# Optimization experiments

Measured on AMD Instinct MI355X. Metric: run time of the kernel, lower is better.

Reference implementation:

```python
import jax, jax.numpy as jnp
import numpy as np

V, D = 100000, 128
B, Q, C, T = 1024, 64, 64, 8


def setup_inputs() -> dict:
    key = jax.random.key(0)
    ks = jax.random.split(key, 9)
    embed = jax.random.normal(ks[0], (V, D), dtype=jnp.float32) * 0.1
    embed = embed.at[0].set(0.0)  # padding_idx=0
    q_ids = jax.random.randint(ks[1], (B, Q), 1, V)
    c_ids = jax.random.randint(ks[2], (B, C, T), 1, V)
    num_qs = jax.random.randint(ks[3], (B,), 1, Q + 1)
    num_cols = jax.random.randint(ks[4], (B,), 1, C + 1)
    W_h = jax.random.normal(ks[5], (5 * D, D), dtype=jnp.float32) * 0.02
    b_h = jnp.zeros((D,), jnp.float32)
    W_o = jax.random.normal(ks[6], (D, 1), dtype=jnp.float32) * 0.02
    b_o = jnp.zeros((1,), jnp.float32)
    return {"q_ids": q_ids, "c_ids": c_ids, "num_qs": num_qs, "num_cols": num_cols,
            "embed": embed, "W_h": W_h, "b_h": b_h, "W_o": W_o, "b_o": b_o}


def _forward(q_ids, c_ids, num_qs, num_cols, embed, W_h, b_h, W_o, b_o):
    d = embed.shape[1]
    # ColumnSummarizer: pad-masked mean over column tokens -> [B, C, D]
    c_tok = embed[c_ids]                       # [B, C, T, D]
    c_mask = (c_ids != 0).astype(c_tok.dtype)  # [B, C, T]
    denom = jnp.maximum(c_mask.sum(-1, keepdims=True), 1.0)
    c_h = (c_tok * c_mask[..., None]).sum(-2) / denom  # [B, C, D]
    # QuestionSummarizer: q_h = token embeddings, q_summary = length-masked mean
    q_h = embed[q_ids]                         # [B, Q, D]
    q_valid = (jnp.arange(q_h.shape[1])[None, :] < num_qs[:, None])  # [B, Q]
    qv = q_valid.astype(q_h.dtype)
    q_summary = (q_h * qv[..., None]).sum(1) / jnp.maximum(
        num_qs[:, None].astype(q_h.dtype), 1.0)  # [B, D]
    # scaled dot-product attention, columns attend over question tokens
    sim = jnp.einsum('bcd,bqd->bcq', c_h, q_h) / jnp.sqrt(jnp.asarray(d, c_h.dtype))
    sim = jnp.where(q_valid[:, None, :], sim, -jnp.inf)  # mask padded q tokens
    att = jax.nn.softmax(sim, axis=-1)                    # [B, C, Q]
    weighted_q = jnp.einsum('bcq,bqd->bcd', att, q_h)     # [B, C, D]
    q_tiled = jnp.broadcast_to(q_summary[:, None, :], c_h.shape)
    feats = jnp.concatenate(
        [q_tiled, c_h, weighted_q, c_h * weighted_q, jnp.abs(c_h - weighted_q)],
        axis=-1)                                           # [B, C, 5D]
    h = jnp.tanh(feats @ W_h + b_h)
    return h @ W_o + b_o                                   # [B, C, 1]


def reference(q_ids, c_ids, num_qs, num_cols, embed, W_h, b_h, W_o, b_o):
    return _forward(q_ids, c_ids, num_qs, num_cols, embed, W_h, b_h, W_o, b_o)
```

## Files before the change

### kernel.cpp

```cpp
#include <hip/hip_runtime.h>


typedef __attribute__((ext_vector_type(8))) short     short8;
typedef __attribute__((ext_vector_type(8))) __bf16    bf16x8;
typedef __attribute__((ext_vector_type(4))) float     f32x4;
typedef __attribute__((ext_vector_type(4))) int       int4v;

#define SWZ8(row, off) ((off) ^ (((row) & 7) << 4))
#define SWZQ(row, off) ((off) ^ (((row) & 7) << 4) ^ ((((row) >> 3) & 3) << 5))

#define CH_OFF  0
#define QH_OFF  16384
#define X_OFF   32768
#define LDS_SIZE 40960

__device__ __forceinline__ unsigned short f2bf(float x) {
    __bf16 h = (__bf16)x;
    return __builtin_bit_cast(unsigned short, h);
}
__device__ __forceinline__ float bf2f(unsigned short u) {
    return __builtin_bit_cast(float, ((unsigned)u) << 16);
}
__device__ __forceinline__ float bflo(unsigned u) {
    return __builtin_bit_cast(float, u << 16);
}
__device__ __forceinline__ float bfhi(unsigned u) {
    return __builtin_bit_cast(float, u & 0xFFFF0000u);
}
__device__ __forceinline__ unsigned pk2(float a, float b) {
    return (unsigned)f2bf(a) | ((unsigned)f2bf(b) << 16);
}
__device__ __forceinline__ f32x4 mfma16(short8 a, short8 b, f32x4 c) {
    return __builtin_amdgcn_mfma_f32_16x16x32_bf16(
        __builtin_bit_cast(bf16x8, a), __builtin_bit_cast(bf16x8, b), c, 0, 0, 0);
}

__global__ __launch_bounds__(256) void el_prep(const float* __restrict__ W_h,
                                               unsigned short* __restrict__ whT) {
    int t = blockIdx.x * 256 + threadIdx.x;
    int k = t >> 7, n = t & 127;
    whT[n * 640 + k] = f2bf(W_h[t]);
}

__global__ __launch_bounds__(256) void el_conv(const float* __restrict__ e,
                                               unsigned short* __restrict__ ebf) {
    long i = ((long)blockIdx.x * 256 + threadIdx.x) * 8;
    f32x4 a = *(const f32x4*)(e + i);
    f32x4 c = *(const f32x4*)(e + i + 4);
    uint4 pk;
    pk.x = pk2(a[0], a[1]); pk.y = pk2(a[2], a[3]);
    pk.z = pk2(c[0], c[1]); pk.w = pk2(c[2], c[3]);
    *(uint4*)(ebf + i) = pk;
}

template <bool BF16E>
__global__ __launch_bounds__(256, 4) void el_main(
    const int* __restrict__ q_ids, const int* __restrict__ c_ids,
    const int* __restrict__ num_qs, const float* __restrict__ emb,
    const unsigned short* __restrict__ ebf,
    const unsigned short* __restrict__ whT,
    unsigned short* __restrict__ qsum_ws,
    const float* __restrict__ b_h,
    const float* __restrict__ W_o, const float* __restrict__ b_o,
    float* __restrict__ out)
{
    __shared__ __align__(16) char smem[LDS_SIZE];
    const int tid = threadIdx.x;
    const int b = blockIdx.x;
    const int nq = num_qs[b] > 0 ? num_qs[b] : 1;

    {
        const int l4 = tid & 15, gg = tid >> 4;
        #pragma unroll 2
        for (int cc = 0; cc < 4; ++cc) {
            const int c = gg + cc * 16;
            const int* idp = c_ids + (((b << 6) + c) << 3);
            int4v i0 = *(const int4v*)idp, i1 = *(const int4v*)(idp + 4);
            int id8[8] = {i0[0], i0[1], i0[2], i0[3], i1[0], i1[1], i1[2], i1[3]};
            int cnt = 0;
            #pragma unroll
            for (int t = 0; t < 8; ++t) cnt += (id8[t] != 0);
            float acc[8] = {0.f,0.f,0.f,0.f,0.f,0.f,0.f,0.f};
            #pragma unroll
            for (int t = 0; t < 8; ++t) {
                if constexpr (BF16E) {
                    uint4 v = *(const uint4*)(ebf + (long)id8[t] * 128 + l4 * 8);
                    acc[0] += bflo(v.x); acc[1] += bfhi(v.x);
                    acc[2] += bflo(v.y); acc[3] += bfhi(v.y);
                    acc[4] += bflo(v.z); acc[5] += bfhi(v.z);
                    acc[6] += bflo(v.w); acc[7] += bfhi(v.w);
                } else {
                    f32x4 lo = *(const f32x4*)(emb + (long)id8[t] * 128 + l4 * 8);
                    f32x4 hi = *(const f32x4*)(emb + (long)id8[t] * 128 + l4 * 8 + 4);
                    acc[0] += lo[0]; acc[1] += lo[1]; acc[2] += lo[2]; acc[3] += lo[3];
                    acc[4] += hi[0]; acc[5] += hi[1]; acc[6] += hi[2]; acc[7] += hi[3];
                }
            }
            float inv = 1.0f / (float)(cnt > 0 ? cnt : 1);
            uint4 pk;
            pk.x = pk2(acc[0]*inv, acc[1]*inv); pk.y = pk2(acc[2]*inv, acc[3]*inv);
            pk.z = pk2(acc[4]*inv, acc[5]*inv); pk.w = pk2(acc[6]*inv, acc[7]*inv);
            *(uint4*)(smem + CH_OFF + SWZ8(c, c * 256 + l4 * 16)) = pk;
        }
        float qa[8] = {0.f,0.f,0.f,0.f,0.f,0.f,0.f,0.f};
        #pragma unroll
        for (int qq = 0; qq < 4; ++qq) {
            const int q = gg + (qq << 4);
            int id = q_ids[(b << 6) + q];
            uint4 v;
            if constexpr (BF16E) {
                v = *(const uint4*)(ebf + (long)id * 128 + l4 * 8);
            } else {
                f32x4 lo = *(const f32x4*)(emb + (long)id * 128 + l4 * 8);
                f32x4 hi = *(const f32x4*)(emb + (long)id * 128 + l4 * 8 + 4);
                v.x = pk2(lo[0], lo[1]); v.y = pk2(lo[2], lo[3]);
                v.z = pk2(hi[0], hi[1]); v.w = pk2(hi[2], hi[3]);
            }
            *(uint4*)(smem + QH_OFF + SWZQ(q, q * 256 + l4 * 16)) = v;
            if (q < nq) {
                qa[0] += bflo(v.x); qa[1] += bfhi(v.x);
                qa[2] += bflo(v.y); qa[3] += bfhi(v.y);
                qa[4] += bflo(v.z); qa[5] += bfhi(v.z);
                qa[6] += bflo(v.w); qa[7] += bfhi(v.w);
            }
        }
        float* qsp = (float*)(smem + X_OFF);
        *(f32x4*)(qsp + gg * 128 + l4 * 8)     = (f32x4){qa[0], qa[1], qa[2], qa[3]};
        *(f32x4*)(qsp + gg * 128 + l4 * 8 + 4) = (f32x4){qa[4], qa[5], qa[6], qa[7]};
    }
    __syncthreads();

    if (tid < 128) {
        const float* qsp = (const float*)(smem + X_OFF);
        float s = 0.f;
        #pragma unroll
        for (int g = 0; g < 16; ++g) s += qsp[g * 128 + tid];
        qsum_ws[(b << 7) + tid] = f2bf(s / (float)nq);
    }
    __syncthreads();

    const int lane = tid & 63, w = tid >> 6;
    const int lr = lane & 15, lg = lane >> 4;

    {
        short8 a[4];
        const int arow = w * 16 + lr;
        #pragma unroll
        for (int s = 0; s < 4; ++s)
            a[s] = *(const short8*)(smem + CH_OFF + SWZ8(arow, arow * 256 + s * 64 + lg * 16));
        f32x4 sim[4];
        #pragma unroll
        for (int ct = 0; ct < 4; ++ct) {
            f32x4 acc = {0.f, 0.f, 0.f, 0.f};
            const int q = ct * 16 + lr;
            #pragma unroll
            for (int s = 0; s < 4; ++s) {
                short8 bf = *(const short8*)(smem + QH_OFF + SWZQ(q, q * 256 + s * 64 + lg * 16));
                acc = mfma16(a[s], bf, acc);
            }
            sim[ct] = acc;
        }
        const float scale = 0.08838834764831845f;
        #pragma unroll
        for (int ct = 0; ct < 4; ++ct) {
            const int q = ct * 16 + lr;
            #pragma unroll
            for (int r = 0; r < 4; ++r)
                sim[ct][r] = (q < nq) ? sim[ct][r] * scale : -3.0e38f;
        }
        float mx[4], sm[4];
        #pragma unroll
        for (int r = 0; r < 4; ++r)
            mx[r] = fmaxf(fmaxf(sim[0][r], sim[1][r]), fmaxf(sim[2][r], sim[3][r]));
        #pragma unroll
        for (int off = 1; off <= 8; off <<= 1)
            #pragma unroll
            for (int r = 0; r < 4; ++r)
                mx[r] = fmaxf(mx[r], __shfl_xor(mx[r], off));
        #pragma unroll
        for (int ct = 0; ct < 4; ++ct)
            #pragma unroll
            for (int r = 0; r < 4; ++r)
                sim[ct][r] = __expf(sim[ct][r] - mx[r]);
        #pragma unroll
        for (int r = 0; r < 4; ++r)
            sm[r] = (sim[0][r] + sim[1][r]) + (sim[2][r] + sim[3][r]);
        #pragma unroll
        for (int off = 1; off <= 8; off <<= 1)
            #pragma unroll
            for (int r = 0; r < 4; ++r)
                sm[r] += __shfl_xor(sm[r], off);
        const int cbase = w * 16 + lg * 4;
        #pragma unroll
        for (int ct = 0; ct < 4; ++ct)
            #pragma unroll
            for (int r = 0; r < 4; ++r) {
                int c = cbase + r, q = ct * 16 + lr;
                *(unsigned short*)(smem + X_OFF + SWZ8(c, c * 128 + q * 2)) =
                    f2bf(sim[ct][r] * (1.0f / sm[r]));
            }
    }
    __syncthreads();

    f32x4 wqa[8];
    {
        short8 pa[2];
        const int arow = w * 16 + lr;
        #pragma unroll
        for (int s = 0; s < 2; ++s)
            pa[s] = *(const short8*)(smem + X_OFF + SWZ8(arow, arow * 128 + s * 64 + lg * 16));
        #pragma unroll
        for (int ct = 0; ct < 8; ++ct) {
            f32x4 acc = {0.f, 0.f, 0.f, 0.f};
            const int d = ct * 16 + lr;
            const int dlx = (d << 1) ^ (lg << 5);
            #pragma unroll
            for (int s = 0; s < 2; ++s) {
                const int qbase = (s << 5) + (lg << 3);
                short8 bf;
                #pragma unroll
                for (int j = 0; j < 8; ++j) {
                    int off = QH_OFF + ((qbase + j) << 8) + (dlx ^ (j << 4));
                    bf[j] = *(const short*)(smem + off);
                }
                acc = mfma16(pa[s], bf, acc);
            }
            wqa[ct] = acc;
        }
    }
    __syncthreads();
    {
        const int cbase = w * 16 + lg * 4;
        #pragma unroll
        for (int ct = 0; ct < 8; ++ct)
            #pragma unroll
            for (int r = 0; r < 4; ++r) {
                int c = cbase + r, d = ct * 16 + lr;
                *(unsigned short*)(smem + QH_OFF + SWZQ(c, c * 256 + d * 2)) =
                    f2bf(wqa[ct][r]);
            }
    }
    __syncthreads();

    {
        f32x4 acc[4][2];
        #pragma unroll
        for (int rt = 0; rt < 4; ++rt) {
            acc[rt][0] = (f32x4){0.f, 0.f, 0.f, 0.f};
            acc[rt][1] = (f32x4){0.f, 0.f, 0.f, 0.f};
        }
        const int n0 = w * 32 + lr, n1 = n0 + 16;
        const int klane = lg * 8;
        short8 qsf[4];
        #pragma unroll
        for (int sk = 0; sk < 4; ++sk)
            qsf[sk] = *(const short8*)(qsum_ws + (b << 7) + sk * 32 + klane);
        const float bh0 = b_h[n0], bh1 = b_h[n1];
        const float wo0 = W_o[n0], wo1 = W_o[n1];

        for (int sk = 0; sk < 4; ++sk) {
            short8 B0[5], B1[5];
            #pragma unroll
            for (int p = 0; p < 5; ++p) {
                B0[p] = *(const short8*)(whT + n0 * 640 + p * 128 + sk * 32 + klane);
                B1[p] = *(const short8*)(whT + n1 * 640 + p * 128 + sk * 32 + klane);
            }
            #pragma unroll
            for (int rt = 0; rt < 4; ++rt) {
                const int row = rt * 16 + lr;
                short8 chf = *(const short8*)(smem + CH_OFF + SWZ8(row, row * 256 + sk * 64 + lg * 16));
                short8 wqf = *(const short8*)(smem + QH_OFF + SWZQ(row, row * 256 + sk * 64 + lg * 16));
                short8 prf, adf;
                #pragma unroll
                for (int e = 0; e < 8; ++e) {
                    float cv = bf2f((unsigned short)chf[e]);
                    float wv = bf2f((unsigned short)wqf[e]);
                    prf[e] = (short)f2bf(cv * wv);
                    adf[e] = (short)f2bf(fabsf(cv - wv));
                }
                acc[rt][0] = mfma16(qsf[sk], B0[0], acc[rt][0]);
                acc[rt][1] = mfma16(qsf[sk], B1[0], acc[rt][1]);
                acc[rt][0] = mfma16(chf,     B0[1], acc[rt][0]);
                acc[rt][1] = mfma16(chf,     B1[1], acc[rt][1]);
                acc[rt][0] = mfma16(wqf,     B0[2], acc[rt][0]);
                acc[rt][1] = mfma16(wqf,     B1[2], acc[rt][1]);
                acc[rt][0] = mfma16(prf,     B0[3], acc[rt][0]);
                acc[rt][1] = mfma16(prf,     B1[3], acc[rt][1]);
                acc[rt][0] = mfma16(adf,     B0[4], acc[rt][0]);
                acc[rt][1] = mfma16(adf,     B1[4], acc[rt][1]);
            }
        }

        #pragma unroll
        for (int rt = 0; rt < 4; ++rt)
            #pragma unroll
            for (int r = 0; r < 4; ++r) {
                float x0 = acc[rt][0][r] + bh0;
                float x1 = acc[rt][1][r] + bh1;
                float t0 = 1.0f - 2.0f / (__expf(2.0f * x0) + 1.0f);
                float t1 = 1.0f - 2.0f / (__expf(2.0f * x1) + 1.0f);
                float po = t0 * wo0 + t1 * wo1;
                #pragma unroll
                for (int off = 1; off <= 8; off <<= 1)
                    po += __shfl_xor(po, off);
                if (lr == 0)
                    *(float*)(smem + X_OFF + (w * 64 + rt * 16 + lg * 4 + r) * 4) = po;
            }
    }
    __syncthreads();

    if (tid < 64) {
        float o = b_o[0];
        #pragma unroll
        for (int w2 = 0; w2 < 4; ++w2)
            o += *(const float*)(smem + X_OFF + (w2 * 64 + tid) * 4);
        out[(b << 6) + tid] = o;
    }
}

extern "C" void kernel_launch(void* const* d_in, const int* in_sizes, int n_in,
                              void* d_out, int out_size, void* d_ws, size_t ws_size,
                              hipStream_t stream) {
    const int*   q_ids  = (const int*)d_in[0];
    const int*   c_ids  = (const int*)d_in[1];
    const int*   num_qs = (const int*)d_in[2];
    const float* embed  = (const float*)d_in[4];
    const float* W_h    = (const float*)d_in[5];
    const float* b_h    = (const float*)d_in[6];
    const float* W_o    = (const float*)d_in[7];
    const float* b_o    = (const float*)d_in[8];
    float*       out    = (float*)d_out;

    unsigned short* whT  = (unsigned short*)d_ws;
    unsigned short* qsum = (unsigned short*)((char*)d_ws + 163840);
    unsigned short* ebf  = (unsigned short*)((char*)d_ws + 425984);

    el_prep<<<320, 256, 0, stream>>>(W_h, whT);

    const bool bf16e = ws_size >= (size_t)(425984 + 100000 * 128 * 2);
    if (bf16e) {
        el_conv<<<6250, 256, 0, stream>>>(embed, ebf);
        el_main<true><<<1024, 256, 0, stream>>>(q_ids, c_ids, num_qs, embed, ebf,
                                                whT, qsum, b_h, W_o, b_o, out);
    } else {
        el_main<false><<<1024, 256, 0, stream>>>(q_ids, c_ids, num_qs, embed, ebf,
                                                 whT, qsum, b_h, W_o, b_o, out);
    }
}
```

Baseline: 151.2 us.

## Add main kernel variant staging attention probs in global workspace to cut LDS

Adds a new main kernel that writes the bf16 attention probabilities and partial question sums to a per-batch global workspace instead of LDS, which shrinks shared memory from 40 KB to 32 KB. It reuses the question-embedding LDS region for weighted_q, fuses the output projection with per-row atomicAdd into an output pre-initialised with b_o, and loads W_h fragments straight from global. The aim is more resident blocks per CU and fewer LDS round trips. In exchange it adds global-memory traffic, extra barriers and atomics, and it only runs when the workspace is large enough.

```diff
diff --git a/kernel.cpp b/kernel.cpp
--- a/kernel.cpp
+++ b/kernel.cpp
@@ -8,6 +8,10 @@
 
 #define SWZ8(row, off) ((off) ^ (((row) & 7) << 4))
 #define SWZQ(row, off) ((off) ^ (((row) & 7) << 4) ^ ((((row) >> 3) & 3) << 5))
+
+#define A_CH   0
+#define A_QH   16384
+#define A_LDS  32768
 
 #define CH_OFF  0
 #define QH_OFF  16384
@@ -53,8 +57,256 @@
     *(uint4*)(ebf + i) = pk;
 }
 
+__global__ __launch_bounds__(256, 4) void el_main_a(
+    const int* __restrict__ q_ids, const int* __restrict__ c_ids,
+    const int* __restrict__ num_qs,
+    const unsigned short* __restrict__ ebf,
+    const unsigned short* __restrict__ whT,
+    unsigned short* __restrict__ qsum_ws,
+    unsigned short* __restrict__ att_ws,
+    const float* __restrict__ b_h,
+    const float* __restrict__ W_o, const float* __restrict__ b_o,
+    float* __restrict__ out)
+{
+    __shared__ __align__(16) char smem[A_LDS];
+    const int tid = threadIdx.x;
+    const int b = blockIdx.x;
+    const int nq = num_qs[b] > 0 ? num_qs[b] : 1;
+    unsigned short* batt = att_ws + (size_t)b * 4096;
+    float* bqp = (float*)batt;
+
+    if (tid < 64) out[(b << 6) + tid] = b_o[0];
+
+    {
+        const int l4 = tid & 15, gg = tid >> 4;
+        #pragma unroll 2
+        for (int cc = 0; cc < 4; ++cc) {
+            const int c = gg + cc * 16;
+            const int* idp = c_ids + (((b << 6) + c) << 3);
+            int4v i0 = *(const int4v*)idp, i1 = *(const int4v*)(idp + 4);
+            int id8[8] = {i0[0], i0[1], i0[2], i0[3], i1[0], i1[1], i1[2], i1[3]};
+            int cnt = 0;
+            #pragma unroll
+            for (int t = 0; t < 8; ++t) cnt += (id8[t] != 0);
+            float acc[8] = {0.f,0.f,0.f,0.f,0.f,0.f,0.f,0.f};
+            #pragma unroll
+            for (int t = 0; t < 8; ++t) {
+                uint4 v = *(const uint4*)(ebf + (long)id8[t] * 128 + l4 * 8);
+                acc[0] += bflo(v.x); acc[1] += bfhi(v.x);
+                acc[2] += bflo(v.y); acc[3] += bfhi(v.y);
+                acc[4] += bflo(v.z); acc[5] += bfhi(v.z);
+                acc[6] += bflo(v.w); acc[7] += bfhi(v.w);
+            }
+            float inv = 1.0f / (float)(cnt > 0 ? cnt : 1);
+            uint4 pk;
+            pk.x = pk2(acc[0]*inv, acc[1]*inv); pk.y = pk2(acc[2]*inv, acc[3]*inv);
+            pk.z = pk2(acc[4]*inv, acc[5]*inv); pk.w = pk2(acc[6]*inv, acc[7]*inv);
+            *(uint4*)(smem + A_CH + SWZ8(c, c * 256 + l4 * 16)) = pk;
+        }
+        float qa[8] = {0.f,0.f,0.f,0.f,0.f,0.f,0.f,0.f};
+        #pragma unroll
+        for (int qq = 0; qq < 4; ++qq) {
+            const int q = gg + (qq << 4);
+            int id = q_ids[(b << 6) + q];
+            uint4 v = *(const uint4*)(ebf + (long)id * 128 + l4 * 8);
+            *(uint4*)(smem + A_QH + SWZQ(q, q * 256 + l4 * 16)) = v;
+            if (q < nq) {
+                qa[0] += bflo(v.x); qa[1] += bfhi(v.x);
+                qa[2] += bflo(v.y); qa[3] += bfhi(v.y);
+                qa[4] += bflo(v.z); qa[5] += bfhi(v.z);
+                qa[6] += bflo(v.w); qa[7] += bfhi(v.w);
+            }
+        }
+        #pragma unroll
+        for (int e = 0; e < 8; ++e) {
+            qa[e] += __shfl_xor(qa[e], 16);
+            qa[e] += __shfl_xor(qa[e], 32);
+        }
+        const int lane = tid & 63, w = tid >> 6;
+        if (lane < 16) {
+            *(f32x4*)(bqp + w * 128 + lane * 8)     = (f32x4){qa[0],qa[1],qa[2],qa[3]};
+            *(f32x4*)(bqp + w * 128 + lane * 8 + 4) = (f32x4){qa[4],qa[5],qa[6],qa[7]};
+        }
+    }
+    __syncthreads();
+
+    if (tid < 128) {
+        float s = bqp[tid] + bqp[128 + tid] + bqp[256 + tid] + bqp[384 + tid];
+        qsum_ws[(b << 7) + tid] = f2bf(s / (float)nq);
+    }
+    __syncthreads();
+
+    const int lane = tid & 63, w = tid >> 6;
+    const int lr = lane & 15, lg = lane >> 4;
+
+    {
+        short8 a[4];
+        const int arow = w * 16 + lr;
+        #pragma unroll
+        for (int s = 0; s < 4; ++s)
+            a[s] = *(const short8*)(smem + A_CH + SWZ8(arow, arow * 256 + s * 64 + lg * 16));
+        f32x4 sim[4];
+        #pragma unroll
+        for (int ct = 0; ct < 4; ++ct) {
+            f32x4 acc = {0.f, 0.f, 0.f, 0.f};
+            const int q = ct * 16 + lr;
+            #pragma unroll
+            for (int s = 0; s < 4; ++s) {
+                short8 bf = *(const short8*)(smem + A_QH + SWZQ(q, q * 256 + s * 64 + lg * 16));
+                acc = mfma16(a[s], bf, acc);
+            }
+            sim[ct] = acc;
+        }
+        const float scale = 0.08838834764831845f;
+        #pragma unroll
+        for (int ct = 0; ct < 4; ++ct) {
+            const int q = ct * 16 + lr;
+            #pragma unroll
+            for (int r = 0; r < 4; ++r)
+                sim[ct][r] = (q < nq) ? sim[ct][r] * scale : -3.0e38f;
+        }
+        float mx[4], sm[4];
+        #pragma unroll
+        for (int r = 0; r < 4; ++r)
+            mx[r] = fmaxf(fmaxf(sim[0][r], sim[1][r]), fmaxf(sim[2][r], sim[3][r]));
+        #pragma unroll
+        for (int off = 1; off <= 8; off <<= 1)
+            #pragma unroll
+            for (int r = 0; r < 4; ++r)
+                mx[r] = fmaxf(mx[r], __shfl_xor(mx[r], off));
+        #pragma unroll
+        for (int ct = 0; ct < 4; ++ct)
+            #pragma unroll
+            for (int r = 0; r < 4; ++r)
+                sim[ct][r] = __expf(sim[ct][r] - mx[r]);
+        #pragma unroll
+        for (int r = 0; r < 4; ++r)
+            sm[r] = (sim[0][r] + sim[1][r]) + (sim[2][r] + sim[3][r]);
+        #pragma unroll
+        for (int off = 1; off <= 8; off <<= 1)
+            #pragma unroll
+            for (int r = 0; r < 4; ++r)
+                sm[r] += __shfl_xor(sm[r], off);
+        const int cbase = w * 16 + lg * 4;
+        #pragma unroll
+        for (int ct = 0; ct < 4; ++ct)
+            #pragma unroll
+            for (int r = 0; r < 4; ++r) {
+                int c = cbase + r, q = ct * 16 + lr;
+                batt[c * 64 + q] = f2bf(sim[ct][r] * (1.0f / sm[r]));
+            }
+    }
+    __syncthreads();
+
+    f32x4 wqa[8];
+    {
+        short8 pa[2];
+        const int prow = w * 16 + lr;
+        #pragma unroll
+        for (int s = 0; s < 2; ++s)
+            pa[s] = *(const short8*)(batt + prow * 64 + s * 32 + lg * 8);
+        #pragma unroll
+        for (int ct = 0; ct < 8; ++ct) {
+            f32x4 acc = {0.f, 0.f, 0.f, 0.f};
+            const int d = ct * 16 + lr;
+            const int dlx = (d << 1) ^ (lg << 5);
+            #pragma unroll
+            for (int s = 0; s < 2; ++s) {
+                const int qbase = (s << 5) + (lg << 3);
+                short8 bf;
+                #pragma unroll
+                for (int j = 0; j < 8; ++j) {
+                    int off = A_QH + ((qbase + j) << 8) + (dlx ^ (j << 4));
+                    bf[j] = *(const short*)(smem + off);
+                }
+                acc = mfma16(pa[s], bf, acc);
+            }
+            wqa[ct] = acc;
+        }
+    }
+    __syncthreads();
+    {
+        const int cbase = w * 16 + lg * 4;
+        #pragma unroll
+        for (int ct = 0; ct < 8; ++ct)
+            #pragma unroll
+            for (int r = 0; r < 4; ++r) {
+                int c = cbase + r, d = ct * 16 + lr;
+                *(unsigned short*)(smem + A_QH + SWZQ(c, c * 256 + d * 2)) =
+                    f2bf(wqa[ct][r]);
+            }
+    }
+    __syncthreads();
+
+    {
+        f32x4 acc[4][2];
+        #pragma unroll
+        for (int rt = 0; rt < 4; ++rt) {
+            acc[rt][0] = (f32x4){0.f, 0.f, 0.f, 0.f};
+            acc[rt][1] = (f32x4){0.f, 0.f, 0.f, 0.f};
+        }
+        const int n0 = w * 32 + lr, n1 = n0 + 16;
+        const int klane = lg * 8;
+        short8 qsf[4];
+        #pragma unroll
+        for (int sk = 0; sk < 4; ++sk)
+            qsf[sk] = *(const short8*)(qsum_ws + (b << 7) + sk * 32 + klane);
+        const float bh0 = b_h[n0], bh1 = b_h[n1];
+        const float wo0 = W_o[n0], wo1 = W_o[n1];
+
+        for (int sk = 0; sk < 4; ++sk) {
+            short8 B0[5], B1[5];
+            #pragma unroll
+            for (int p = 0; p < 5; ++p) {
+                B0[p] = *(const short8*)(whT + n0 * 640 + p * 128 + sk * 32 + klane);
+                B1[p] = *(const short8*)(whT + n1 * 640 + p * 128 + sk * 32 + klane);
+            }
+            #pragma unroll
+            for (int rt = 0; rt < 4; ++rt) {
+                const int row = rt * 16 + lr;
+                short8 chf = *(const short8*)(smem + A_CH + SWZ8(row, row * 256 + sk * 64 + lg * 16));
+                short8 wqf = *(const short8*)(smem + A_QH + SWZQ(row, row * 256 + sk * 64 + lg * 16));
+                short8 prf, adf;
+                #pragma unroll
+                for (int e = 0; e < 8; ++e) {
+                    float cv = bf2f((unsigned short)chf[e]);
+                    float wv = bf2f((unsigned short)wqf[e]);
+                    prf[e] = (short)f2bf(cv * wv);
+                    adf[e] = (short)f2bf(fabsf(cv - wv));
+                }
+                acc[rt][0] = mfma16(qsf[sk], B0[0], acc[rt][0]);
+                acc[rt][1] = mfma16(qsf[sk], B1[0], acc[rt][1]);
+                acc[rt][0] = mfma16(chf,     B0[1], acc[rt][0]);
+                acc[rt][1] = mfma16(chf,     B1[1], acc[rt][1]);
+                acc[rt][0] = mfma16(wqf,     B0[2], acc[rt][0]);
+                acc[rt][1] = mfma16(wqf,     B1[2], acc[rt][1]);
+                acc[rt][0] = mfma16(prf,     B0[3], acc[rt][0]);
+                acc[rt][1] = mfma16(prf,     B1[3], acc[rt][1]);
+                acc[rt][0] = mfma16(adf,     B0[4], acc[rt][0]);
+                acc[rt][1] = mfma16(adf,     B1[4], acc[rt][1]);
+            }
+        }
+
+        #pragma unroll
+        for (int rt = 0; rt < 4; ++rt)
+            #pragma unroll
+            for (int r = 0; r < 4; ++r) {
+                float x0 = acc[rt][0][r] + bh0;
+                float x1 = acc[rt][1][r] + bh1;
+                float t0 = 1.0f - 2.0f / (__expf(2.0f * x0) + 1.0f);
+                float t1 = 1.0f - 2.0f / (__expf(2.0f * x1) + 1.0f);
+                float po = t0 * wo0 + t1 * wo1;
+                #pragma unroll
+                for (int off = 1; off <= 8; off <<= 1)
+                    po += __shfl_xor(po, off);
+                if (lr == 0)
+                    atomicAdd(out + (b << 6) + rt * 16 + lg * 4 + r, po);
+            }
+    }
+}
+
 template <bool BF16E>
-__global__ __launch_bounds__(256, 4) void el_main(
+__global__ __launch_bounds__(256, 4) void el_main_b(
     const int* __restrict__ q_ids, const int* __restrict__ c_ids,
     const int* __restrict__ num_qs, const float* __restrict__ emb,
     const unsigned short* __restrict__ ebf,
@@ -331,19 +583,26 @@
     const float* b_o    = (const float*)d_in[8];
     float*       out    = (float*)d_out;
 
+    const size_t EBF_OFF = 425984;
+    const size_t EBF_END = EBF_OFF + (size_t)100000 * 128 * 2;
+    const size_t ATT_END = EBF_END + (size_t)1024 * 4096 * 2;
     unsigned short* whT  = (unsigned short*)d_ws;
     unsigned short* qsum = (unsigned short*)((char*)d_ws + 163840);
-    unsigned short* ebf  = (unsigned short*)((char*)d_ws + 425984);
+    unsigned short* ebf  = (unsigned short*)((char*)d_ws + EBF_OFF);
+    unsigned short* attw = (unsigned short*)((char*)d_ws + EBF_END);
 
     el_prep<<<320, 256, 0, stream>>>(W_h, whT);
 
-    const bool bf16e = ws_size >= (size_t)(425984 + 100000 * 128 * 2);
-    if (bf16e) {
+    if (ws_size >= ATT_END) {
         el_conv<<<6250, 256, 0, stream>>>(embed, ebf);
-        el_main<true><<<1024, 256, 0, stream>>>(q_ids, c_ids, num_qs, embed, ebf,
-                                                whT, qsum, b_h, W_o, b_o, out);
+        el_main_a<<<1024, 256, 0, stream>>>(q_ids, c_ids, num_qs, ebf, whT,
+                                            qsum, attw, b_h, W_o, b_o, out);
+    } else if (ws_size >= EBF_END) {
+        el_conv<<<6250, 256, 0, stream>>>(embed, ebf);
+        el_main_b<true><<<1024, 256, 0, stream>>>(q_ids, c_ids, num_qs, embed, ebf,
+                                                  whT, qsum, b_h, W_o, b_o, out);
     } else {
-        el_main<false><<<1024, 256, 0, stream>>>(q_ids, c_ids, num_qs, embed, ebf,
-                                                 whT, qsum, b_h, W_o, b_o, out);
-    }
-}
+        el_main_b<false><<<1024, 256, 0, stream>>>(q_ids, c_ids, num_qs, embed, ebf,
+                                                   whT, qsum, b_h, W_o, b_o, out);
+    }
+}
```

Result: slower. 156.2 us (+3.3%).

## Split each batch row across two blocks by column halves

Applied to the files above, without the earlier changes.

Launches two blocks per batch element, each handling 32 of the 64 columns, which halves the LDS footprint and doubles the grid for more parallelism and occupancy. The question summary is now reduced with wave shuffles and kept in LDS instead of a global workspace round-trip. Index loads are hoisted ahead of the gathers. The cost is that both blocks redundantly gather and stage all 64 question embeddings, and half the waves idle during the similarity/softmax stage.

```diff
diff --git a/kernel.cpp b/kernel.cpp
--- a/kernel.cpp
+++ b/kernel.cpp
@@ -9,10 +9,12 @@
 #define SWZ8(row, off) ((off) ^ (((row) & 7) << 4))
 #define SWZQ(row, off) ((off) ^ (((row) & 7) << 4) ^ ((((row) >> 3) & 3) << 5))
 
-#define CH_OFF  0
-#define QH_OFF  16384
-#define X_OFF   32768
-#define LDS_SIZE 40960
+#define H_CH   0
+#define H_QH   8192
+#define H_X    24576
+#define H_QSP  28672
+#define H_QS   30720
+#define H_LDS  30976
 
 __device__ __forceinline__ unsigned short f2bf(float x) {
     __bf16 h = (__bf16)x;
@@ -54,29 +56,40 @@
 }
 
 template <bool BF16E>
-__global__ __launch_bounds__(256, 4) void el_main(
+__global__ __launch_bounds__(256, 4) void el_half(
     const int* __restrict__ q_ids, const int* __restrict__ c_ids,
     const int* __restrict__ num_qs, const float* __restrict__ emb,
     const unsigned short* __restrict__ ebf,
     const unsigned short* __restrict__ whT,
-    unsigned short* __restrict__ qsum_ws,
     const float* __restrict__ b_h,
     const float* __restrict__ W_o, const float* __restrict__ b_o,
     float* __restrict__ out)
 {
-    __shared__ __align__(16) char smem[LDS_SIZE];
+    __shared__ __align__(16) char smem[H_LDS];
     const int tid = threadIdx.x;
-    const int b = blockIdx.x;
+    const int hb = blockIdx.x, b = hb >> 1, half = hb & 1;
     const int nq = num_qs[b] > 0 ? num_qs[b] : 1;
+    float* qsp = (float*)(smem + H_QSP);
+    unsigned short* qs = (unsigned short*)(smem + H_QS);
 
     {
         const int l4 = tid & 15, gg = tid >> 4;
-        #pragma unroll 2
-        for (int cc = 0; cc < 4; ++cc) {
-            const int c = gg + cc * 16;
-            const int* idp = c_ids + (((b << 6) + c) << 3);
-            int4v i0 = *(const int4v*)idp, i1 = *(const int4v*)(idp + 4);
-            int id8[8] = {i0[0], i0[1], i0[2], i0[3], i1[0], i1[1], i1[2], i1[3]};
+        const int cg = (b << 6) + (half << 5) + gg;
+        int4v ci[2][2];
+        ci[0][0] = *(const int4v*)(c_ids + (cg << 3));
+        ci[0][1] = *(const int4v*)(c_ids + (cg << 3) + 4);
+        ci[1][0] = *(const int4v*)(c_ids + ((cg + 16) << 3));
+        ci[1][1] = *(const int4v*)(c_ids + ((cg + 16) << 3) + 4);
+        int qid[4];
+        #pragma unroll
+        for (int qq = 0; qq < 4; ++qq)
+            qid[qq] = q_ids[(b << 6) + gg + (qq << 4)];
+
+        #pragma unroll
+        for (int cc = 0; cc < 2; ++cc) {
+            const int cl = gg + cc * 16;
+            int id8[8] = {ci[cc][0][0], ci[cc][0][1], ci[cc][0][2], ci[cc][0][3],
+                          ci[cc][1][0], ci[cc][1][1], ci[cc][1][2], ci[cc][1][3]};
             int cnt = 0;
             #pragma unroll
             for (int t = 0; t < 8; ++t) cnt += (id8[t] != 0);
@@ -100,54 +113,53 @@
             uint4 pk;
             pk.x = pk2(acc[0]*inv, acc[1]*inv); pk.y = pk2(acc[2]*inv, acc[3]*inv);
             pk.z = pk2(acc[4]*inv, acc[5]*inv); pk.w = pk2(acc[6]*inv, acc[7]*inv);
-            *(uint4*)(smem + CH_OFF + SWZ8(c, c * 256 + l4 * 16)) = pk;
+            *(uint4*)(smem + H_CH + SWZ8(cl, cl * 256 + l4 * 16)) = pk;
         }
         float qa[8] = {0.f,0.f,0.f,0.f,0.f,0.f,0.f,0.f};
         #pragma unroll
         for (int qq = 0; qq < 4; ++qq) {
             const int q = gg + (qq << 4);
-            int id = q_ids[(b << 6) + q];
             uint4 v;
+            float e8[8];
             if constexpr (BF16E) {
-                v = *(const uint4*)(ebf + (long)id * 128 + l4 * 8);
+                v = *(const uint4*)(ebf + (long)qid[qq] * 128 + l4 * 8);
+                e8[0]=bflo(v.x); e8[1]=bfhi(v.x); e8[2]=bflo(v.y); e8[3]=bfhi(v.y);
+                e8[4]=bflo(v.z); e8[5]=bfhi(v.z); e8[6]=bflo(v.w); e8[7]=bfhi(v.w);
             } else {
-                f32x4 lo = *(const f32x4*)(emb + (long)id * 128 + l4 * 8);
-                f32x4 hi = *(const f32x4*)(emb + (long)id * 128 + l4 * 8 + 4);
+                f32x4 lo = *(const f32x4*)(emb + (long)qid[qq] * 128 + l4 * 8);
+                f32x4 hi = *(const f32x4*)(emb + (long)qid[qq] * 128 + l4 * 8 + 4);
+                e8[0]=lo[0]; e8[1]=lo[1]; e8[2]=lo[2]; e8[3]=lo[3];
+                e8[4]=hi[0]; e8[5]=hi[1]; e8[6]=hi[2]; e8[7]=hi[3];
                 v.x = pk2(lo[0], lo[1]); v.y = pk2(lo[2], lo[3]);
                 v.z = pk2(hi[0], hi[1]); v.w = pk2(hi[2], hi[3]);
             }
-            *(uint4*)(smem + QH_OFF + SWZQ(q, q * 256 + l4 * 16)) = v;
-            if (q < nq) {
-                qa[0] += bflo(v.x); qa[1] += bfhi(v.x);
-                qa[2] += bflo(v.y); qa[3] += bfhi(v.y);
-                qa[4] += bflo(v.z); qa[5] += bfhi(v.z);
-                qa[6] += bflo(v.w); qa[7] += bfhi(v.w);
-            }
-        }
-        float* qsp = (float*)(smem + X_OFF);
-        *(f32x4*)(qsp + gg * 128 + l4 * 8)     = (f32x4){qa[0], qa[1], qa[2], qa[3]};
-        *(f32x4*)(qsp + gg * 128 + l4 * 8 + 4) = (f32x4){qa[4], qa[5], qa[6], qa[7]};
-    }
-    __syncthreads();
-
-    if (tid < 128) {
-        const float* qsp = (const float*)(smem + X_OFF);
-        float s = 0.f;
-        #pragma unroll
-        for (int g = 0; g < 16; ++g) s += qsp[g * 128 + tid];
-        qsum_ws[(b << 7) + tid] = f2bf(s / (float)nq);
+            *(uint4*)(smem + H_QH + SWZQ(q, q * 256 + l4 * 16)) = v;
+            if (q < nq)
+                #pragma unroll
+                for (int e = 0; e < 8; ++e) qa[e] += e8[e];
+        }
+        #pragma unroll
+        for (int e = 0; e < 8; ++e) {
+            qa[e] += __shfl_xor(qa[e], 16);
+            qa[e] += __shfl_xor(qa[e], 32);
+        }
+        const int lane = tid & 63, w = tid >> 6;
+        if (lane < 16) {
+            *(f32x4*)(qsp + w * 128 + lane * 8)     = (f32x4){qa[0],qa[1],qa[2],qa[3]};
+            *(f32x4*)(qsp + w * 128 + lane * 8 + 4) = (f32x4){qa[4],qa[5],qa[6],qa[7]};
+        }
     }
     __syncthreads();
 
     const int lane = tid & 63, w = tid >> 6;
     const int lr = lane & 15, lg = lane >> 4;
 
-    {
+    if (w < 2) {
         short8 a[4];
         const int arow = w * 16 + lr;
         #pragma unroll
         for (int s = 0; s < 4; ++s)
-            a[s] = *(const short8*)(smem + CH_OFF + SWZ8(arow, arow * 256 + s * 64 + lg * 16));
+            a[s] = *(const short8*)(smem + H_CH + SWZ8(arow, arow * 256 + s * 64 + lg * 16));
         f32x4 sim[4];
         #pragma unroll
         for (int ct = 0; ct < 4; ++ct) {
@@ -155,7 +167,7 @@
             const int q = ct * 16 + lr;
             #pragma unroll
             for (int s = 0; s < 4; ++s) {
-                short8 bf = *(const short8*)(smem + QH_OFF + SWZQ(q, q * 256 + s * 64 + lg * 16));
+                short8 bf = *(const short8*)(smem + H_QH + SWZQ(q, q * 256 + s * 64 + lg * 16));
                 acc = mfma16(a[s], bf, acc);
             }
             sim[ct] = acc;
@@ -196,23 +208,32 @@
             #pragma unroll
             for (int r = 0; r < 4; ++r) {
                 int c = cbase + r, q = ct * 16 + lr;
-                *(unsigned short*)(smem + X_OFF + SWZ8(c, c * 128 + q * 2)) =
+                *(unsigned short*)(smem + H_X + SWZ8(c, c * 128 + q * 2)) =
                     f2bf(sim[ct][r] * (1.0f / sm[r]));
             }
-    }
-    __syncthreads();
-
-    f32x4 wqa[8];
+    } else if (w == 2) {
+        const float invq = 1.0f / (float)nq;
+        #pragma unroll
+        for (int h = 0; h < 2; ++h) {
+            int d = lane + h * 64;
+            float s = qsp[d] + qsp[128 + d] + qsp[256 + d] + qsp[384 + d];
+            qs[d] = f2bf(s * invq);
+        }
+    }
+    __syncthreads();
+
+    f32x4 wqa[4];
+    const int ctile = w & 1, ct0 = (w >> 1) * 4;
     {
         short8 pa[2];
-        const int arow = w * 16 + lr;
+        const int arow = ctile * 16 + lr;
         #pragma unroll
         for (int s = 0; s < 2; ++s)
-            pa[s] = *(const short8*)(smem + X_OFF + SWZ8(arow, arow * 128 + s * 64 + lg * 16));
-        #pragma unroll
-        for (int ct = 0; ct < 8; ++ct) {
+            pa[s] = *(const short8*)(smem + H_X + SWZ8(arow, arow * 128 + s * 64 + lg * 16));
+        #pragma unroll
+        for (int ct = 0; ct < 4; ++ct) {
             f32x4 acc = {0.f, 0.f, 0.f, 0.f};
-            const int d = ct * 16 + lr;
+            const int d = (ct0 + ct) * 16 + lr;
             const int dlx = (d << 1) ^ (lg << 5);
             #pragma unroll
             for (int s = 0; s < 2; ++s) {
@@ -220,7 +241,7 @@
                 short8 bf;
                 #pragma unroll
                 for (int j = 0; j < 8; ++j) {
-                    int off = QH_OFF + ((qbase + j) << 8) + (dlx ^ (j << 4));
+                    int off = H_QH + ((qbase + j) << 8) + (dlx ^ (j << 4));
                     bf[j] = *(const short*)(smem + off);
                 }
                 acc = mfma16(pa[s], bf, acc);
@@ -230,22 +251,22 @@
     }
     __syncthreads();
     {
-        const int cbase = w * 16 + lg * 4;
-        #pragma unroll
-        for (int ct = 0; ct < 8; ++ct)
+        const int cbase = ctile * 16 + lg * 4;
+        #pragma unroll
+        for (int ct = 0; ct < 4; ++ct)
             #pragma unroll
             for (int r = 0; r < 4; ++r) {
-                int c = cbase + r, d = ct * 16 + lr;
-                *(unsigned short*)(smem + QH_OFF + SWZQ(c, c * 256 + d * 2)) =
+                int c = cbase + r, d = (ct0 + ct) * 16 + lr;
+                *(unsigned short*)(smem + H_QH + SWZQ(c, c * 256 + d * 2)) =
                     f2bf(wqa[ct][r]);
             }
     }
     __syncthreads();
 
     {
-        f32x4 acc[4][2];
-        #pragma unroll
-        for (int rt = 0; rt < 4; ++rt) {
+        f32x4 acc[2][2];
+        #pragma unroll
+        for (int rt = 0; rt < 2; ++rt) {
             acc[rt][0] = (f32x4){0.f, 0.f, 0.f, 0.f};
             acc[rt][1] = (f32x4){0.f, 0.f, 0.f, 0.f};
         }
@@ -254,7 +275,7 @@
         short8 qsf[4];
         #pragma unroll
         for (int sk = 0; sk < 4; ++sk)
-            qsf[sk] = *(const short8*)(qsum_ws + (b << 7) + sk * 32 + klane);
+            qsf[sk] = *(const short8*)(qs + sk * 32 + klane);
         const float bh0 = b_h[n0], bh1 = b_h[n1];
         const float wo0 = W_o[n0], wo1 = W_o[n1];
 
@@ -266,10 +287,10 @@
                 B1[p] = *(const short8*)(whT + n1 * 640 + p * 128 + sk * 32 + klane);
             }
             #pragma unroll
-            for (int rt = 0; rt < 4; ++rt) {
+            for (int rt = 0; rt < 2; ++rt) {
                 const int row = rt * 16 + lr;
-                short8 chf = *(const short8*)(smem + CH_OFF + SWZ8(row, row * 256 + sk * 64 + lg * 16));
-                short8 wqf = *(const short8*)(smem + QH_OFF + SWZQ(row, row * 256 + sk * 64 + lg * 16));
+                short8 chf = *(const short8*)(smem + H_CH + SWZ8(row, row * 256 + sk * 64 + lg * 16));
+                short8 wqf = *(const short8*)(smem + H_QH + SWZQ(row, row * 256 + sk * 64 + lg * 16));
                 short8 prf, adf;
                 #pragma unroll
                 for (int e = 0; e < 8; ++e) {
@@ -292,7 +313,7 @@
         }
 
         #pragma unroll
-        for (int rt = 0; rt < 4; ++rt)
+        for (int rt = 0; rt < 2; ++rt)
             #pragma unroll
             for (int r = 0; r < 4; ++r) {
                 float x0 = acc[rt][0][r] + bh0;
@@ -304,17 +325,17 @@
                 for (int off = 1; off <= 8; off <<= 1)
                     po += __shfl_xor(po, off);
                 if (lr == 0)
-                    *(float*)(smem + X_OFF + (w * 64 + rt * 16 + lg * 4 + r) * 4) = po;
-            }
-    }
-    __syncthreads();
-
-    if (tid < 64) {
+                    *(float*)(smem + H_X + (w * 32 + rt * 16 + lg * 4 + r) * 4) = po;
+            }
+    }
+    __syncthreads();
+
+    if (tid < 32) {
         float o = b_o[0];
         #pragma unroll
         for (int w2 = 0; w2 < 4; ++w2)
-            o += *(const float*)(smem + X_OFF + (w2 * 64 + tid) * 4);
-        out[(b << 6) + tid] = o;
+            o += *(const float*)(smem + H_X + (w2 * 32 + tid) * 4);
+        out[(b << 6) + (half << 5) + tid] = o;
     }
 }
 
@@ -331,19 +352,19 @@
     const float* b_o    = (const float*)d_in[8];
     float*       out    = (float*)d_out;
 
-    unsigned short* whT  = (unsigned short*)d_ws;
-    unsigned short* qsum = (unsigned short*)((char*)d_ws + 163840);
-    unsigned short* ebf  = (unsigned short*)((char*)d_ws + 425984);
+    const size_t EBF_OFF = 163840;
+    const size_t EBF_END = EBF_OFF + (size_t)100000 * 128 * 2;
+    unsigned short* whT = (unsigned short*)d_ws;
+    unsigned short* ebf = (unsigned short*)((char*)d_ws + EBF_OFF);
 
     el_prep<<<320, 256, 0, stream>>>(W_h, whT);
 
-    const bool bf16e = ws_size >= (size_t)(425984 + 100000 * 128 * 2);
-    if (bf16e) {
+    if (ws_size >= EBF_END) {
         el_conv<<<6250, 256, 0, stream>>>(embed, ebf);
-        el_main<true><<<1024, 256, 0, stream>>>(q_ids, c_ids, num_qs, embed, ebf,
-                                                whT, qsum, b_h, W_o, b_o, out);
+        el_half<true><<<2048, 256, 0, stream>>>(q_ids, c_ids, num_qs, embed, ebf,
+                                                whT, b_h, W_o, b_o, out);
     } else {
-        el_main<false><<<1024, 256, 0, stream>>>(q_ids, c_ids, num_qs, embed, ebf,
-                                                 whT, qsum, b_h, W_o, b_o, out);
-    }
-}
+        el_half<false><<<2048, 256, 0, stream>>>(q_ids, c_ids, num_qs, embed, ebf,
+                                                 whT, b_h, W_o, b_o, out);
+    }
+}
```

Result: slower. 161.9 us (+7.1%).

## Drop bf16 embedding conversion pass and gather fp32 rows with batched loads

Applied to the files above, without the earlier changes.

Removes the separate kernel that converted the whole 100k x 128 embedding table to bf16 on every call, and instead gathers the needed fp32 rows directly inside the main kernel. All id loads and the 8 token-row loads per column are issued up front into registers so the gather has more memory-level parallelism. The occupancy hint drops from 4 to 3 blocks per CU to leave room for the extra live registers. This trades a full-table read and write for twice the bytes per gathered row.

```diff
diff --git a/kernel.cpp b/kernel.cpp
--- a/kernel.cpp
+++ b/kernel.cpp
@@ -20,12 +20,6 @@
 }
 __device__ __forceinline__ float bf2f(unsigned short u) {
     return __builtin_bit_cast(float, ((unsigned)u) << 16);
-}
-__device__ __forceinline__ float bflo(unsigned u) {
-    return __builtin_bit_cast(float, u << 16);
-}
-__device__ __forceinline__ float bfhi(unsigned u) {
-    return __builtin_bit_cast(float, u & 0xFFFF0000u);
 }
 __device__ __forceinline__ unsigned pk2(float a, float b) {
     return (unsigned)f2bf(a) | ((unsigned)f2bf(b) << 16);
@@ -42,22 +36,9 @@
     whT[n * 640 + k] = f2bf(W_h[t]);
 }
 
-__global__ __launch_bounds__(256) void el_conv(const float* __restrict__ e,
-                                               unsigned short* __restrict__ ebf) {
-    long i = ((long)blockIdx.x * 256 + threadIdx.x) * 8;
-    f32x4 a = *(const f32x4*)(e + i);
-    f32x4 c = *(const f32x4*)(e + i + 4);
-    uint4 pk;
-    pk.x = pk2(a[0], a[1]); pk.y = pk2(a[2], a[3]);
-    pk.z = pk2(c[0], c[1]); pk.w = pk2(c[2], c[3]);
-    *(uint4*)(ebf + i) = pk;
-}
-
-template <bool BF16E>
-__global__ __launch_bounds__(256, 4) void el_main(
+__global__ __launch_bounds__(256, 3) void el_main(
     const int* __restrict__ q_ids, const int* __restrict__ c_ids,
     const int* __restrict__ num_qs, const float* __restrict__ emb,
-    const unsigned short* __restrict__ ebf,
     const unsigned short* __restrict__ whT,
     unsigned short* __restrict__ qsum_ws,
     const float* __restrict__ b_h,
@@ -71,57 +52,64 @@
 
     {
         const int l4 = tid & 15, gg = tid >> 4;
+        int4v ci[4][2];
+        #pragma unroll
+        for (int cc = 0; cc < 4; ++cc) {
+            const int* idp = c_ids + (((b << 6) + gg + cc * 16) << 3);
+            ci[cc][0] = *(const int4v*)idp;
+            ci[cc][1] = *(const int4v*)(idp + 4);
+        }
+        int qid[4];
+        #pragma unroll
+        for (int qq = 0; qq < 4; ++qq)
+            qid[qq] = q_ids[(b << 6) + gg + (qq << 4)];
+
+        f32x4 qlo[4], qhi[4];
+        #pragma unroll
+        for (int qq = 0; qq < 4; ++qq) {
+            const float* p = emb + (long)qid[qq] * 128 + l4 * 8;
+            qlo[qq] = *(const f32x4*)p;
+            qhi[qq] = *(const f32x4*)(p + 4);
+        }
+
         #pragma unroll 2
         for (int cc = 0; cc < 4; ++cc) {
             const int c = gg + cc * 16;
-            const int* idp = c_ids + (((b << 6) + c) << 3);
-            int4v i0 = *(const int4v*)idp, i1 = *(const int4v*)(idp + 4);
-            int id8[8] = {i0[0], i0[1], i0[2], i0[3], i1[0], i1[1], i1[2], i1[3]};
+            int id8[8] = {ci[cc][0][0], ci[cc][0][1], ci[cc][0][2], ci[cc][0][3],
+                          ci[cc][1][0], ci[cc][1][1], ci[cc][1][2], ci[cc][1][3]};
+            f32x4 vlo[8], vhi[8];
+            #pragma unroll
+            for (int t = 0; t < 8; ++t) {
+                const float* p = emb + (long)id8[t] * 128 + l4 * 8;
+                vlo[t] = *(const f32x4*)p;
+                vhi[t] = *(const f32x4*)(p + 4);
+            }
             int cnt = 0;
             #pragma unroll
             for (int t = 0; t < 8; ++t) cnt += (id8[t] != 0);
-            float acc[8] = {0.f,0.f,0.f,0.f,0.f,0.f,0.f,0.f};
-            #pragma unroll
-            for (int t = 0; t < 8; ++t) {
-                if constexpr (BF16E) {
-                    uint4 v = *(const uint4*)(ebf + (long)id8[t] * 128 + l4 * 8);
-                    acc[0] += bflo(v.x); acc[1] += bfhi(v.x);
-                    acc[2] += bflo(v.y); acc[3] += bfhi(v.y);
-                    acc[4] += bflo(v.z); acc[5] += bfhi(v.z);
-                    acc[6] += bflo(v.w); acc[7] += bfhi(v.w);
-                } else {
-                    f32x4 lo = *(const f32x4*)(emb + (long)id8[t] * 128 + l4 * 8);
-                    f32x4 hi = *(const f32x4*)(emb + (long)id8[t] * 128 + l4 * 8 + 4);
-                    acc[0] += lo[0]; acc[1] += lo[1]; acc[2] += lo[2]; acc[3] += lo[3];
-                    acc[4] += hi[0]; acc[5] += hi[1]; acc[6] += hi[2]; acc[7] += hi[3];
-                }
-            }
+            f32x4 alo = {0.f,0.f,0.f,0.f}, ahi = {0.f,0.f,0.f,0.f};
+            #pragma unroll
+            for (int t = 0; t < 8; ++t) { alo += vlo[t]; ahi += vhi[t]; }
             float inv = 1.0f / (float)(cnt > 0 ? cnt : 1);
             uint4 pk;
-            pk.x = pk2(acc[0]*inv, acc[1]*inv); pk.y = pk2(acc[2]*inv, acc[3]*inv);
-            pk.z = pk2(acc[4]*inv, acc[5]*inv); pk.w = pk2(acc[6]*inv, acc[7]*inv);
+            pk.x = pk2(alo[0]*inv, alo[1]*inv); pk.y = pk2(alo[2]*inv, alo[3]*inv);
+            pk.z = pk2(ahi[0]*inv, ahi[1]*inv); pk.w = pk2(ahi[2]*inv, ahi[3]*inv);
             *(uint4*)(smem + CH_OFF + SWZ8(c, c * 256 + l4 * 16)) = pk;
         }
+
         float qa[8] = {0.f,0.f,0.f,0.f,0.f,0.f,0.f,0.f};
         #pragma unroll
         for (int qq = 0; qq < 4; ++qq) {
             const int q = gg + (qq << 4);
-            int id = q_ids[(b << 6) + q];
             uint4 v;
-            if constexpr (BF16E) {
-                v = *(const uint4*)(ebf + (long)id * 128 + l4 * 8);
-            } else {
-                f32x4 lo = *(const f32x4*)(emb + (long)id * 128 + l4 * 8);
-                f32x4 hi = *(const f32x4*)(emb + (long)id * 128 + l4 * 8 + 4);
-                v.x = pk2(lo[0], lo[1]); v.y = pk2(lo[2], lo[3]);
-                v.z = pk2(hi[0], hi[1]); v.w = pk2(hi[2], hi[3]);
-            }
+            v.x = pk2(qlo[qq][0], qlo[qq][1]); v.y = pk2(qlo[qq][2], qlo[qq][3]);
+            v.z = pk2(qhi[qq][0], qhi[qq][1]); v.w = pk2(qhi[qq][2], qhi[qq][3]);
             *(uint4*)(smem + QH_OFF + SWZQ(q, q * 256 + l4 * 16)) = v;
             if (q < nq) {
-                qa[0] += bflo(v.x); qa[1] += bfhi(v.x);
-                qa[2] += bflo(v.y); qa[3] += bfhi(v.y);
-                qa[4] += bflo(v.z); qa[5] += bfhi(v.z);
-                qa[6] += bflo(v.w); qa[7] += bfhi(v.w);
+                qa[0] += qlo[qq][0]; qa[1] += qlo[qq][1];
+                qa[2] += qlo[qq][2]; qa[3] += qlo[qq][3];
+                qa[4] += qhi[qq][0]; qa[5] += qhi[qq][1];
+                qa[6] += qhi[qq][2]; qa[7] += qhi[qq][3];
             }
         }
         float* qsp = (float*)(smem + X_OFF);
@@ -333,17 +321,8 @@
 
     unsigned short* whT  = (unsigned short*)d_ws;
     unsigned short* qsum = (unsigned short*)((char*)d_ws + 163840);
-    unsigned short* ebf  = (unsigned short*)((char*)d_ws + 425984);
 
     el_prep<<<320, 256, 0, stream>>>(W_h, whT);
-
-    const bool bf16e = ws_size >= (size_t)(425984 + 100000 * 128 * 2);
-    if (bf16e) {
-        el_conv<<<6250, 256, 0, stream>>>(embed, ebf);
-        el_main<true><<<1024, 256, 0, stream>>>(q_ids, c_ids, num_qs, embed, ebf,
-                                                whT, qsum, b_h, W_o, b_o, out);
-    } else {
-        el_main<false><<<1024, 256, 0, stream>>>(q_ids, c_ids, num_qs, embed, ebf,
-                                                 whT, qsum, b_h, W_o, b_o, out);
-    }
-}
+    el_main<<<1024, 256, 0, stream>>>(q_ids, c_ids, num_qs, embed,
+                                      whT, qsum, b_h, W_o, b_o, out);
+}
```

Result: no change. 150.5 us (-0.4%).
